# Performance work log

Hardware: AMD Instinct MI355X
Metric: run time of the kernel (lower is better)

## Reference

```python
import jax, jax.numpy as jnp
import numpy as np

C = 1024      # channels
K = 7         # kernel_size
G = 1         # groups (G>1 crashes in the original torch code; see notes)
GC = C // G   # group_channels
OFFSET_SCALE = 2.0
LN_EPS = 1e-5


def setup_inputs() -> dict:
    key = jax.random.key(0)
    ks = jax.random.split(key, 8)
    N, L = 4, 2048
    s = 1.0 / np.sqrt(C)
    x = jax.random.normal(ks[0], (N, L, C), jnp.float32)
    Wi = jax.random.normal(ks[1], (C, C), jnp.float32) * s
    bi = jnp.zeros((C,), jnp.float32)
    dw_w = jax.random.normal(ks[2], (C, 1, 3), jnp.float32) * 0.5   # depthwise conv kernel (O, I/g=1, W)
    dw_b = jnp.zeros((C,), jnp.float32)
    ln_g = jnp.ones((C,), jnp.float32)
    ln_b = jnp.zeros((C,), jnp.float32)
    Wo = jax.random.normal(ks[3], (G * K, C), jnp.float32) * 0.02   # offset head (nonzero to exercise gather)
    bo = jnp.zeros((G * K,), jnp.float32)
    Wm = jax.random.normal(ks[4], (G * K, C), jnp.float32) * 0.02   # mask head
    bm = jnp.zeros((G * K,), jnp.float32)
    Wout = jax.random.normal(ks[5], (C, C), jnp.float32) * s
    bout = jnp.zeros((C,), jnp.float32)
    return {"x": x, "Wi": Wi, "bi": bi, "dw_w": dw_w, "dw_b": dw_b,
            "ln_g": ln_g, "ln_b": ln_b, "Wo": Wo, "bo": bo,
            "Wm": Wm, "bm": bm, "Wout": Wout, "bout": bout}


def _forward(x, Wi, bi, dw_w, dw_b, ln_g, ln_b, Wo, bo, Wm, bm, Wout, bout):
    N, L, Cc = x.shape
    dt = x.dtype
    # input projection
    x_proj = x @ Wi.T + bi                                  # [N,L,C]
    # depthwise conv (k=3, pad=1, groups=C) -> LayerNorm(C) -> GELU(exact)
    y = jax.lax.conv_general_dilated(
        x.transpose(0, 2, 1), dw_w, window_strides=(1,), padding=((1, 1),),
        dimension_numbers=("NCH", "OIH", "NCH"), feature_group_count=Cc)
    x_dw = y.transpose(0, 2, 1) + dw_b                       # [N,L,C]
    mu = x_dw.mean(-1, keepdims=True)
    var = ((x_dw - mu) ** 2).mean(-1, keepdims=True)
    x_dw = (x_dw - mu) * jax.lax.rsqrt(var + LN_EPS) * ln_g + ln_b
    x_dw = jax.nn.gelu(x_dw, approximate=False)
    # dynamic offsets and sampling mask
    offsets = (x_dw @ Wo.T + bo).reshape(N, L, G, K) * OFFSET_SCALE
    mask = jax.nn.softmax((x_dw @ Wm.T + bm).reshape(N, L, G, K), axis=-1)
    mask = jnp.nan_to_num(mask, nan=0.0)
    # absolute sampling positions
    ref_off = jnp.linspace(-(K // 2), K // 2, K).astype(dt)          # [K]
    pos = jnp.arange(L, dtype=dt)[None, :, None, None]               # [1,L,1,1]
    abs_pos = pos + ref_off[None, None, None, :] + offsets           # [N,L,G,K]
    apc = jnp.clip(abs_pos, 0.0, L - 1)
    p_floor = jnp.clip(apc.astype(jnp.int32), 0, L - 1)
    p_ceil = jnp.clip(p_floor + 1, 0, L - 1)
    w_ceil = apc - p_floor.astype(dt)
    w_floor = 1.0 - w_ceil
    valid = jnp.logical_not((abs_pos < 0) | (abs_pos > L - 1)).astype(dt)
    w_floor = w_floor * valid
    w_ceil = w_ceil * valid
    # gather + bilinear blend (G=1: each sample index grabs the full C channels)
    idx_f = p_floor.reshape(N, -1)[:, :, None]                       # [N, L*G*K, 1]
    idx_c = p_ceil.reshape(N, -1)[:, :, None]
    v_floor = jnp.take_along_axis(x_proj, idx_f, axis=1).reshape(N, L, G, K, GC)
    v_ceil = jnp.take_along_axis(x_proj, idx_c, axis=1).reshape(N, L, G, K, GC)
    sampled = v_floor * w_floor[..., None] + v_ceil * w_ceil[..., None]
    out = (sampled * mask[..., None]).sum(axis=3).reshape(N, L, Cc)  # sum over K
    return out @ Wout.T + bout


def reference(x, Wi, bi, dw_w, dw_b, ln_g, ln_b, Wo, bo, Wm, bm, Wout, bout):
    return _forward(x, Wi, bi, dw_w, dw_b, ln_g, ln_b, Wo, bo, Wm, bm, Wout, bout)
```

## Files before the change

### kernel.cpp

```cpp
#include <hip/hip_runtime.h>
#include <hip/hip_bf16.h>
#include <cstdint>

#define C_DIM 1024
#define L_DIM 2048
#define N_DIM 4
#define M_DIM (N_DIM * L_DIM)

typedef __attribute__((ext_vector_type(8))) short frag8;
typedef __attribute__((ext_vector_type(4)))  float f32x4;
typedef __attribute__((ext_vector_type(16))) float f32x16;

__device__ __forceinline__ void gl_lds16(const void* g, void* l) {
  __builtin_amdgcn_global_load_lds((const __attribute__((address_space(1))) void*)g,
                                   (__attribute__((address_space(3))) void*)l,
                                   16, 0, 0);
}
__device__ __forceinline__ void store_out(float* Y, size_t idx, float v) { Y[idx] = v; }
__device__ __forceinline__ void store_out(__hip_bfloat16* Y, size_t idx, float v) {
  Y[idx] = __float2bfloat16(v);
}
__device__ __forceinline__ float4 ldbf4(const __hip_bfloat16* p) {
  union { short4 s; __hip_bfloat16 h[4]; } u; u.s = *(const short4*)p;
  return make_float4((float)u.h[0], (float)u.h[1], (float)u.h[2], (float)u.h[3]);
}
__device__ __forceinline__ void stbf4(__hip_bfloat16* p, float4 v) {
  union { short4 s; __hip_bfloat16 h[4]; } u;
  u.h[0] = __float2bfloat16(v.x); u.h[1] = __float2bfloat16(v.y);
  u.h[2] = __float2bfloat16(v.z); u.h[3] = __float2bfloat16(v.w);
  *(short4*)p = u.s;
}
__device__ __forceinline__ float gelu_fast(float t) {
  const float t3 = t * t * t;
  const float ns = -1.5957691216f * t - 0.0713548163f * t3;
  return t / (1.f + __expf(ns));
}

__global__ __launch_bounds__(256)
void cvt_f32_bf16(const float* __restrict__ in, __hip_bfloat16* __restrict__ out, int n8) {
  const int i = blockIdx.x * 256 + threadIdx.x;
  if (i >= n8) return;
  const float4 a = *(const float4*)(in + (size_t)i * 8);
  const float4 b = *(const float4*)(in + (size_t)i * 8 + 4);
  union { __hip_bfloat16 h[8]; int4 q; } u;
  u.h[0] = __float2bfloat16(a.x); u.h[1] = __float2bfloat16(a.y);
  u.h[2] = __float2bfloat16(a.z); u.h[3] = __float2bfloat16(a.w);
  u.h[4] = __float2bfloat16(b.x); u.h[5] = __float2bfloat16(b.y);
  u.h[6] = __float2bfloat16(b.z); u.h[7] = __float2bfloat16(b.w);
  *(int4*)(out + (size_t)i * 8) = u.q;
}

__global__ __launch_bounds__(256)
void cvt_two_f32_bf16(const float* __restrict__ inA, __hip_bfloat16* __restrict__ outA,
                      const float* __restrict__ inB, __hip_bfloat16* __restrict__ outB,
                      int n8each) {
  int i = blockIdx.x * 256 + threadIdx.x;
  const float* in; __hip_bfloat16* out;
  if (i < n8each) { in = inA; out = outA; }
  else            { in = inB; out = outB; i -= n8each; }
  if (i >= n8each) return;
  const float4 a = *(const float4*)(in + (size_t)i * 8);
  const float4 b = *(const float4*)(in + (size_t)i * 8 + 4);
  union { __hip_bfloat16 h[8]; int4 q; } u;
  u.h[0] = __float2bfloat16(a.x); u.h[1] = __float2bfloat16(a.y);
  u.h[2] = __float2bfloat16(a.z); u.h[3] = __float2bfloat16(a.w);
  u.h[4] = __float2bfloat16(b.x); u.h[5] = __float2bfloat16(b.y);
  u.h[6] = __float2bfloat16(b.z); u.h[7] = __float2bfloat16(b.w);
  *(int4*)(out + (size_t)i * 8) = u.q;
}

template <typename TY>
__global__ __launch_bounds__(256, 2)
void gemm_db(const __hip_bfloat16* __restrict__ X,
             const __hip_bfloat16* __restrict__ W,
             const float* __restrict__ bias,
             TY* __restrict__ Y, int M, int N, int K,
             const float* __restrict__ sArr, const float* __restrict__ bvec)
{
  __shared__ __hip_bfloat16 As[2][2][128 * 32];
  __shared__ __hip_bfloat16 Bs[2][2][128 * 32];
  const int tid  = threadIdx.x;
  const int lane = tid & 63;
  const int wave = tid >> 6;
  const int bm = blockIdx.x * 128;
  const int bn = blockIdx.y * 128;
  const int wr = (wave >> 1) * 64;
  const int wc = (wave & 1) * 64;
  const int srow  = tid >> 2;
  const int skoff = (tid & 3) * 8;

  const __hip_bfloat16* gA0 = X + (size_t)(bm + srow) * K + skoff;
  const __hip_bfloat16* gA1 = X + (size_t)(bm + 64 + srow) * K + skoff;
  const __hip_bfloat16* gB0 = W + (size_t)(bn + srow) * K + skoff;
  const __hip_bfloat16* gB1 = W + (size_t)(bn + 64 + srow) * K + skoff;

  f32x16 acc[2][2] = {};
  const int arow  = lane & 31;
  const int akoff = (lane >> 5) * 8;

#define STAGE(k0, buf)                                        \
  do {                                                        \
    gl_lds16(gA0 + (k0),      &As[buf][0][tid * 8]);          \
    gl_lds16(gA1 + (k0),      &As[buf][0][2048 + tid * 8]);   \
    gl_lds16(gA0 + (k0) + 32, &As[buf][1][tid * 8]);          \
    gl_lds16(gA1 + (k0) + 32, &As[buf][1][2048 + tid * 8]);   \
    gl_lds16(gB0 + (k0),      &Bs[buf][0][tid * 8]);          \
    gl_lds16(gB1 + (k0),      &Bs[buf][0][2048 + tid * 8]);   \
    gl_lds16(gB0 + (k0) + 32, &Bs[buf][1][tid * 8]);          \
    gl_lds16(gB1 + (k0) + 32, &Bs[buf][1][2048 + tid * 8]);   \
  } while (0)

  STAGE(0, 0);
  __syncthreads();
  const int iters = K / 64;
  for (int it = 0; it < iters; ++it) {
    const int cur = it & 1;
    if (it + 1 < iters) STAGE((it + 1) * 64, cur ^ 1);

#pragma unroll
    for (int p = 0; p < 2; ++p)
#pragma unroll
      for (int h = 0; h < 2; ++h) {
        const frag8 a0 = *(const frag8*)&As[cur][p][(wr + arow) * 32 + h * 16 + akoff];
        const frag8 a1 = *(const frag8*)&As[cur][p][(wr + 32 + arow) * 32 + h * 16 + akoff];
        const frag8 b0 = *(const frag8*)&Bs[cur][p][(wc + arow) * 32 + h * 16 + akoff];
        const frag8 b1 = *(const frag8*)&Bs[cur][p][(wc + 32 + arow) * 32 + h * 16 + akoff];
        acc[0][0] = __builtin_amdgcn_mfma_f32_32x32x16_bf16(a0, b0, acc[0][0], 0, 0, 0);
        acc[0][1] = __builtin_amdgcn_mfma_f32_32x32x16_bf16(a0, b1, acc[0][1], 0, 0, 0);
        acc[1][0] = __builtin_amdgcn_mfma_f32_32x32x16_bf16(a1, b0, acc[1][0], 0, 0, 0);
        acc[1][1] = __builtin_amdgcn_mfma_f32_32x32x16_bf16(a1, b1, acc[1][1], 0, 0, 0);
      }
    __syncthreads();
  }
#undef STAGE

#pragma unroll
  for (int i = 0; i < 2; i++)
#pragma unroll
    for (int j = 0; j < 2; j++) {
      const int col = bn + wc + j * 32 + (lane & 31);
      const float bv  = bias ? bias[col] : 0.f;
      const float bvv = (sArr && bvec) ? bvec[col] : 0.f;
#pragma unroll
      for (int r = 0; r < 16; r++) {
        const int row = bm + wr + i * 32 + (r & 3) + 8 * (r >> 2) + 4 * (lane >> 5);
        float extra = bv;
        if (sArr) extra += sArr[row] * bvv;
        store_out(Y, (size_t)row * N + col, acc[i][j][r] + extra);
      }
    }
}

struct Ld8f { float4 a, b; };
struct Ld8b { int4 a; };
__device__ __forceinline__ Ld8f ld8(const float* p) {
  return { *(const float4*)p, *(const float4*)(p + 4) };
}
__device__ __forceinline__ Ld8b ld8(const __hip_bfloat16* p) { return { *(const int4*)p }; }
__device__ __forceinline__ void st8(__hip_bfloat16* l, const Ld8f& v) {
  union { __hip_bfloat16 h[8]; int4 q; } u;
  u.h[0] = __float2bfloat16(v.a.x); u.h[1] = __float2bfloat16(v.a.y);
  u.h[2] = __float2bfloat16(v.a.z); u.h[3] = __float2bfloat16(v.a.w);
  u.h[4] = __float2bfloat16(v.b.x); u.h[5] = __float2bfloat16(v.b.y);
  u.h[6] = __float2bfloat16(v.b.z); u.h[7] = __float2bfloat16(v.b.w);
  *(int4*)l = u.q;
}
__device__ __forceinline__ void st8(__hip_bfloat16* l, const Ld8b& v) { *(int4*)l = v.a; }

template <typename TX, typename TY>
__global__ __launch_bounds__(256, 2)
void gemm_nt(const TX* __restrict__ X, const float* __restrict__ W,
             const float* __restrict__ bias, TY* __restrict__ Y, int M, int N, int K)
{
  __shared__ __hip_bfloat16 As[128 * 32];
  __shared__ __hip_bfloat16 Bs[128 * 32];
  const int tid  = threadIdx.x;
  const int lane = tid & 63;
  const int wave = tid >> 6;
  const int bm = blockIdx.x * 128;
  const int bn = blockIdx.y * 128;
  const int wr = (wave >> 1) * 64;
  const int wc = (wave & 1) * 64;
  const int srow  = tid >> 2;
  const int skoff = (tid & 3) * 8;

  f32x4 acc[4][4] = {};
  const TX*    gA0 = X + (size_t)(bm + srow) * K + skoff;
  const TX*    gA1 = X + (size_t)(bm + 64 + srow) * K + skoff;
  const float* gB0 = W + (size_t)(bn + srow) * K + skoff;
  const float* gB1 = W + (size_t)(bn + 64 + srow) * K + skoff;
  const int arow  = lane & 15;
  const int akoff = (lane >> 4) * 8;

  for (int k0 = 0; k0 < K; k0 += 32) {
    const auto va0 = ld8(gA0 + k0);
    const auto va1 = ld8(gA1 + k0);
    const auto vb0 = ld8(gB0 + k0);
    const auto vb1 = ld8(gB1 + k0);
    __syncthreads();
    st8(&As[srow * 32 + skoff],        va0);
    st8(&As[(64 + srow) * 32 + skoff], va1);
    st8(&Bs[srow * 32 + skoff],        vb0);
    st8(&Bs[(64 + srow) * 32 + skoff], vb1);
    __syncthreads();

    frag8 a[4], b[4];
#pragma unroll
    for (int i = 0; i < 4; i++)
      a[i] = *(const frag8*)&As[(wr + i * 16 + arow) * 32 + akoff];
#pragma unroll
    for (int j = 0; j < 4; j++)
      b[j] = *(const frag8*)&Bs[(wc + j * 16 + arow) * 32 + akoff];
#pragma unroll
    for (int i = 0; i < 4; i++)
#pragma unroll
      for (int j = 0; j < 4; j++)
        acc[i][j] = __builtin_amdgcn_mfma_f32_16x16x32_bf16(a[i], b[j], acc[i][j], 0, 0, 0);
  }
#pragma unroll
  for (int i = 0; i < 4; i++)
#pragma unroll
    for (int j = 0; j < 4; j++) {
      const int col = bn + wc + j * 16 + (lane & 15);
      const float bv = bias[col];
#pragma unroll
      for (int r = 0; r < 4; r++) {
        const int row = bm + wr + i * 16 + (lane >> 4) * 4 + r;
        store_out(Y, (size_t)row * N + col, acc[i][j][r] + bv);
      }
    }
}

__global__ __launch_bounds__(256, 2)
void pre_aux(const float* __restrict__ x,
             const float* __restrict__ dw_w, const float* __restrict__ dw_b,
             const float* __restrict__ ln_g, const float* __restrict__ ln_b,
             const float* __restrict__ Wo,   const float* __restrict__ bo,
             const float* __restrict__ Wm,   const float* __restrict__ bmb,
             const float* __restrict__ Wi,   const float* __restrict__ Wout,
             const float* __restrict__ bi,
             __hip_bfloat16* __restrict__ xbb,
             float* __restrict__ coef,
             __hip_bfloat16* __restrict__ WiT,
             __hip_bfloat16* __restrict__ Woutb,
             float* __restrict__ bvec)
{
  __shared__ float smem[16384];
  const int blk  = blockIdx.x;
  const int tid  = threadIdx.x;
  const int lane = tid & 63;
  const int wid  = tid >> 6;

  if (blk < 256) {
    float (*tile)[65] = (float(*)[65])smem;
    const int bi_ = blk >> 4;
    const int bj  = blk & 15;
    const int r   = tid >> 2;
    const int c0  = (tid & 3) * 16;
    const float* src = Wi + (size_t)(bi_ * 64 + r) * C_DIM + bj * 64 + c0;
    *(float4*)&tile[r][c0]      = *(const float4*)(src);
    *(float4*)&tile[r][c0 + 4]  = *(const float4*)(src + 4);
    *(float4*)&tile[r][c0 + 8]  = *(const float4*)(src + 8);
    *(float4*)&tile[r][c0 + 12] = *(const float4*)(src + 12);
    __syncthreads();
    __hip_bfloat16* dst = WiT + (size_t)(bj * 64 + r) * C_DIM + bi_ * 64 + c0;
    union { __hip_bfloat16 h[16]; int4 q[2]; } u;
#pragma unroll
    for (int i = 0; i < 16; i++) u.h[i] = __float2bfloat16(tile[c0 + i][r]);
    *(int4*)(dst)     = u.q[0];
    *(int4*)(dst + 8) = u.q[1];
    return;
  }
  if (blk < 512) {
    const size_t base = ((size_t)(blk - 256) * 256 + tid) * 16;
#pragma unroll
    for (int h = 0; h < 2; h++) {
      const float4 a = *(const float4*)(Wout + base + h * 8);
      const float4 c = *(const float4*)(Wout + base + h * 8 + 4);
      union { __hip_bfloat16 h8[8]; int4 q; } u;
      u.h8[0] = __float2bfloat16(a.x); u.h8[1] = __float2bfloat16(a.y);
      u.h8[2] = __float2bfloat16(a.z); u.h8[3] = __float2bfloat16(a.w);
      u.h8[4] = __float2bfloat16(c.x); u.h8[5] = __float2bfloat16(c.y);
      u.h8[6] = __float2bfloat16(c.z); u.h8[7] = __float2bfloat16(c.w);
      *(int4*)(Woutb + base + h * 8) = u.q;
    }
    return;
  }
  if (blk < 768) {
    const int row = (blk - 512) * 4 + wid;
    const float* wr_ = Wout + (size_t)row * C_DIM;
    float s = 0.f;
#pragma unroll
    for (int c = 0; c < 4; c++) {
      const int j = c * 256 + lane * 4;
      const float4 w  = *(const float4*)(wr_ + j);
      const float4 bb = *(const float4*)(bi + j);
      s += w.x * bb.x + w.y * bb.y + w.z * bb.z + w.w * bb.w;
    }
#pragma unroll
    for (int m = 1; m < 64; m <<= 1) s += __shfl_xor(s, m);
    if (lane == 0) bvec[row] = s;
    return;
  }

  float* sWo  = smem;
  float* sWm  = smem + 7168;
  float* slng = smem + 14336;
  float* slnb = smem + 15360;

#pragma unroll
  for (int i = 0; i < 7; i++)
    gl_lds16(Wo + (size_t)(i * 256 + tid) * 4, &sWo[(i * 256 + tid) * 4]);
#pragma unroll
  for (int i = 0; i < 7; i++)
    gl_lds16(Wm + (size_t)(i * 256 + tid) * 4, &sWm[(i * 256 + tid) * 4]);
  gl_lds16(ln_g + (size_t)tid * 4, &slng[tid * 4]);
  gl_lds16(ln_b + (size_t)tid * 4, &slnb[tid * 4]);
  __syncthreads();

  const int b    = blk - 768;
  const int bs   = (b & 7) * 64 + (b >> 3);
  const int row0 = bs * 16 + wid * 4;
  const int l0   = row0 & (L_DIM - 1);

  const float* xr = x + (size_t)row0 * C_DIM;

  float4 v[4][4];
#pragma unroll
  for (int j = 0; j < 4; j++) {
    const int c4 = j * 256 + lane * 4;
    float4 xv[6];
#pragma unroll
    for (int m = 0; m < 6; m++) {
      const int lm = l0 + m - 1;
      if (lm >= 0 && lm < L_DIM)
        xv[m] = *(const float4*)(xr + ((long)m - 1) * C_DIM + c4);
      else
        xv[m] = make_float4(0.f, 0.f, 0.f, 0.f);
    }
#pragma unroll
    for (int r = 0; r < 4; r++)
      stbf4(xbb + (size_t)(row0 + r) * C_DIM + c4, xv[r + 1]);

    const float4 w0 = *(const float4*)(dw_w + (size_t)c4 * 3);
    const float4 w1 = *(const float4*)(dw_w + (size_t)c4 * 3 + 4);
    const float4 w2 = *(const float4*)(dw_w + (size_t)c4 * 3 + 8);
    const float4 bb = *(const float4*)(dw_b + c4);
#pragma unroll
    for (int r = 0; r < 4; r++) {
      const float4 xm = xv[r], x0 = xv[r + 1], xq = xv[r + 2];
      v[r][j].x = xm.x * w0.x + x0.x * w0.y + xq.x * w0.z + bb.x;
      v[r][j].y = xm.y * w0.w + x0.y * w1.x + xq.y * w1.y + bb.y;
      v[r][j].z = xm.z * w1.z + x0.z * w1.w + xq.z * w2.x + bb.z;
      v[r][j].w = xm.w * w2.y + x0.w * w2.z + xq.w * w2.w + bb.w;
    }
  }

  float mu[4], rstd[4];
#pragma unroll
  for (int r = 0; r < 4; r++) {
    float s1 = 0.f, s2 = 0.f;
#pragma unroll
    for (int j = 0; j < 4; j++) {
      s1 += v[r][j].x + v[r][j].y + v[r][j].z + v[r][j].w;
      s2 += v[r][j].x * v[r][j].x + v[r][j].y * v[r][j].y
          + v[r][j].z * v[r][j].z + v[r][j].w * v[r][j].w;
    }
    const float t1 = s1 + __shfl_xor(s1, 32);
    const float t2 = s2 + __shfl_xor(s2, 32);
    float cc = (lane < 32) ? t1 : t2;
#pragma unroll
    for (int m = 16; m >= 1; m >>= 1) cc += __shfl_xor(cc, m);
    const float dd = __shfl_xor(cc, 32);
    const float S1 = (lane < 32) ? cc : dd;
    const float S2 = (lane < 32) ? dd : cc;
    mu[r]   = S1 * (1.f / C_DIM);
    rstd[r] = rsqrtf(S2 * (1.f / C_DIM) - mu[r] * mu[r] + 1e-5f);
  }

  float po[4][7] = {}, pm[4][7] = {};
#pragma unroll
  for (int j = 0; j < 4; j++) {
    const int c4 = j * 256 + lane * 4;
    const float4 gg = *(const float4*)&slng[c4];
    const float4 bb = *(const float4*)&slnb[c4];
    float4 g[4];
#pragma unroll
    for (int r = 0; r < 4; r++) {
      g[r].x = gelu_fast((v[r][j].x - mu[r]) * rstd[r] * gg.x + bb.x);
      g[r].y = gelu_fast((v[r][j].y - mu[r]) * rstd[r] * gg.y + bb.y);
      g[r].z = gelu_fast((v[r][j].z - mu[r]) * rstd[r] * gg.z + bb.z);
      g[r].w = gelu_fast((v[r][j].w - mu[r]) * rstd[r] * gg.w + bb.w);
    }
#pragma unroll
    for (int k = 0; k < 7; k++) {
      const float4 wo = *(const float4*)&sWo[k * 1024 + c4];
      const float4 wm = *(const float4*)&sWm[k * 1024 + c4];
#pragma unroll
      for (int r = 0; r < 4; r++) {
        po[r][k] += g[r].x * wo.x + g[r].y * wo.y + g[r].z * wo.z + g[r].w * wo.w;
        pm[r][k] += g[r].x * wm.x + g[r].y * wm.y + g[r].z * wm.z + g[r].w * wm.w;
      }
    }
  }

  float poS[4][7], pmS[4][7];
#pragma unroll
  for (int r = 0; r < 4; r++)
#pragma unroll
    for (int k = 0; k < 7; k++) {
      const float tp = po[r][k] + __shfl_xor(po[r][k], 32);
      const float tm = pm[r][k] + __shfl_xor(pm[r][k], 32);
      float cc = (lane < 32) ? tp : tm;
#pragma unroll
      for (int m = 16; m >= 1; m >>= 1) cc += __shfl_xor(cc, m);
      const float dd = __shfl_xor(cc, 32);
      poS[r][k] = (lane < 32) ? cc : dd;
      pmS[r][k] = (lane < 32) ? dd : cc;
    }

#pragma unroll
  for (int r = 0; r < 4; r++) {
    float lg[7], mx = -1e30f;
#pragma unroll
    for (int k = 0; k < 7; k++) { lg[k] = pmS[r][k] + bmb[k]; mx = fmaxf(mx, lg[k]); }
    float se = 0.f, e[7];
#pragma unroll
    for (int k = 0; k < 7; k++) { e[k] = __expf(lg[k] - mx); se += e[k]; }
    const float inv = 1.f / se;
    const int l = l0 + r;

    if (lane == r) {
      float pk[32];
#pragma unroll
      for (int k = 0; k < 7; k++) {
        const float msk = e[k] * inv;
        const float off = (poS[r][k] + bo[k]) * 2.0f;
        const float ap  = (float)l + (float)(k - 3) + off;
        const float apc = fminf(fmaxf(ap, 0.f), (float)(L_DIM - 1));
        int f = (int)apc;
        int c = f + 1; if (c > L_DIM - 1) c = L_DIM - 1;
        const float w1  = apc - (float)f;
        const float val = (ap < 0.f || ap > (float)(L_DIM - 1)) ? 0.f : 1.f;
        pk[k]      = (1.f - w1) * val * msk;
        pk[8 + k]  = w1 * val * msk;
        pk[16 + k] = (float)f;
        pk[24 + k] = (float)c;
      }
      pk[7] = pk[15] = pk[23] = pk[31] = 0.f;
      float* cr = coef + (size_t)(row0 + r) * 32;
#pragma unroll
      for (int q = 0; q < 8; q++)
        *(float4*)(cr + q * 4) = make_float4(pk[q*4], pk[q*4+1], pk[q*4+2], pk[q*4+3]);
    }
  }
}

__global__ __launch_bounds__(512, 2)
void wcomb_gather(const __hip_bfloat16* __restrict__ Woutb,
                  const __hip_bfloat16* __restrict__ WiT,
                  __hip_bfloat16* __restrict__ Wcb,
                  const float* __restrict__ coef,
                  const __hip_bfloat16* __restrict__ xbb,
                  __hip_bfloat16* __restrict__ gb,
                  float* __restrict__ sArr)
{
  __shared__ __hip_bfloat16 As[2][2][128 * 32];
  __shared__ __hip_bfloat16 Bs[2][2][128 * 32];
  const int tid  = threadIdx.x;
  const int lane = tid & 63;
  const int wid  = tid >> 6;

  if (blockIdx.x < 64) {
    if (wid >= 4) {
      for (int i = 0; i < 17; i++) __syncthreads();
      return;
    }
    const int bm = (int)(blockIdx.x >> 3) * 128;
    const int bn = (int)(blockIdx.x & 7) * 128;
    const int wr = (wid >> 1) * 64;
    const int wc = (wid & 1) * 64;
    const int srow  = tid >> 2;
    const int skoff = (tid & 3) * 8;
    const int K = C_DIM;

    const __hip_bfloat16* gA0 = Woutb + (size_t)(bm + srow) * K + skoff;
    const __hip_bfloat16* gA1 = Woutb + (size_t)(bm + 64 + srow) * K + skoff;
    const __hip_bfloat16* gB0 = WiT   + (size_t)(bn + srow) * K + skoff;
    const __hip_bfloat16* gB1 = WiT   + (size_t)(bn + 64 + srow) * K + skoff;

    f32x16 acc[2][2] = {};
    const int arow  = lane & 31;
    const int akoff = (lane >> 5) * 8;

#define WSTAGE(k0, buf)                                       \
  do {                                                        \
    gl_lds16(gA0 + (k0),      &As[buf][0][tid * 8]);          \
    gl_lds16(gA1 + (k0),      &As[buf][0][2048 + tid * 8]);   \
    gl_lds16(gA0 + (k0) + 32, &As[buf][1][tid * 8]);          \
    gl_lds16(gA1 + (k0) + 32, &As[buf][1][2048 + tid * 8]);   \
    gl_lds16(gB0 + (k0),      &Bs[buf][0][tid * 8]);          \
    gl_lds16(gB1 + (k0),      &Bs[buf][0][2048 + tid * 8]);   \
    gl_lds16(gB0 + (k0) + 32, &Bs[buf][1][tid * 8]);          \
    gl_lds16(gB1 + (k0) + 32, &Bs[buf][1][2048 + tid * 8]);   \
  } while (0)

    WSTAGE(0, 0);
    __syncthreads();
    for (int it = 0; it < 16; ++it) {
      const int cur = it & 1;
      if (it + 1 < 16) WSTAGE((it + 1) * 64, cur ^ 1);
#pragma unroll
      for (int p = 0; p < 2; ++p)
#pragma unroll
        for (int h = 0; h < 2; ++h) {
          const frag8 a0 = *(const frag8*)&As[cur][p][(wr + arow) * 32 + h * 16 + akoff];
          const frag8 a1 = *(const frag8*)&As[cur][p][(wr + 32 + arow) * 32 + h * 16 + akoff];
          const frag8 b0 = *(const frag8*)&Bs[cur][p][(wc + arow) * 32 + h * 16 + akoff];
          const frag8 b1 = *(const frag8*)&Bs[cur][p][(wc + 32 + arow) * 32 + h * 16 + akoff];
          acc[0][0] = __builtin_amdgcn_mfma_f32_32x32x16_bf16(a0, b0, acc[0][0], 0, 0, 0);
          acc[0][1] = __builtin_amdgcn_mfma_f32_32x32x16_bf16(a0, b1, acc[0][1], 0, 0, 0);
          acc[1][0] = __builtin_amdgcn_mfma_f32_32x32x16_bf16(a1, b0, acc[1][0], 0, 0, 0);
          acc[1][1] = __builtin_amdgcn_mfma_f32_32x32x16_bf16(a1, b1, acc[1][1], 0, 0, 0);
        }
      __syncthreads();
    }
#undef WSTAGE

#pragma unroll
    for (int i = 0; i < 2; i++)
#pragma unroll
      for (int j = 0; j < 2; j++) {
        const int col = bn + wc + j * 32 + (lane & 31);
#pragma unroll
        for (int r = 0; r < 16; r++) {
          const int row = bm + wr + i * 32 + (r & 3) + 8 * (r >> 2) + 4 * (lane >> 5);
          Wcb[(size_t)row * C_DIM + col] = __float2bfloat16(acc[i][j][r]);
        }
      }
    return;
  }

  const int b   = (int)blockIdx.x - 64;
  const int bs  = (b & 7) * 128 + (b >> 3);
  const int row = bs * 8 + wid;
  const int n   = row >> 11;

  const float* cr = coef + (size_t)row * 32;
  const float4 q0 = *(const float4*)(cr);
  const float4 q1 = *(const float4*)(cr + 4);
  const float4 q2 = *(const float4*)(cr + 8);
  const float4 q3 = *(const float4*)(cr + 12);
  const float4 q4 = *(const float4*)(cr + 16);
  const float4 q5 = *(const float4*)(cr + 20);
  const float4 q6 = *(const float4*)(cr + 24);
  const float4 q7 = *(const float4*)(cr + 28);

  const float wf[7] = {q0.x, q0.y, q0.z, q0.w, q1.x, q1.y, q1.z};
  const float wc[7] = {q2.x, q2.y, q2.z, q2.w, q3.x, q3.y, q3.z};
  const int   pf[7] = {(int)q4.x, (int)q4.y, (int)q4.z, (int)q4.w, (int)q5.x, (int)q5.y, (int)q5.z};
  const int   pc[7] = {(int)q6.x, (int)q6.y, (int)q6.z, (int)q6.w, (int)q7.x, (int)q7.y, (int)q7.z};

  if (lane == 0) {
    sArr[row] = q0.x + q0.y + q0.z + q0.w + q1.x + q1.y + q1.z
              + q2.x + q2.y + q2.z + q2.w + q3.x + q3.y + q3.z;
  }

  const __hip_bfloat16* xpn = xbb + ((size_t)n * L_DIM) * C_DIM;
  __hip_bfloat16* so = gb + (size_t)row * C_DIM;

#pragma unroll
  for (int j = 0; j < 2; j++) {
    const int c8 = j * 512 + lane * 8;
    float a[8] = {0.f, 0.f, 0.f, 0.f, 0.f, 0.f, 0.f, 0.f};
#pragma unroll
    for (int k = 0; k < 7; k++) {
      union { int4 q; __hip_bfloat16 h[8]; } uf, uc;
      uf.q = *(const int4*)(xpn + (size_t)pf[k] * C_DIM + c8);
      uc.q = *(const int4*)(xpn + (size_t)pc[k] * C_DIM + c8);
#pragma unroll
      for (int t = 0; t < 8; t++)
        a[t] += wf[k] * (float)uf.h[t] + wc[k] * (float)uc.h[t];
    }
    union { int4 q; __hip_bfloat16 h[8]; } uo;
#pragma unroll
    for (int t = 0; t < 8; t++) uo.h[t] = __float2bfloat16(a[t]);
    *(int4*)(so + c8) = uo.q;
  }
}

__global__ __launch_bounds__(256)
void mid_fused_v4(const float* __restrict__ x,
                  const float* __restrict__ dw_w, const float* __restrict__ dw_b,
                  const float* __restrict__ ln_g, const float* __restrict__ ln_b,
                  const float* __restrict__ Wo,   const float* __restrict__ bo,
                  const float* __restrict__ Wm,   const float* __restrict__ bmb,
                  const __hip_bfloat16* __restrict__ xp,
                  __hip_bfloat16* __restrict__ smp)
{
  const int b    = blockIdx.x;
  const int bs   = (b & 7) * 256 + (b >> 3);
  const int wid  = threadIdx.x >> 6;
  const int lane = threadIdx.x & 63;
  const int row  = bs * 4 + wid;
  const int l    = row & (L_DIM - 1);
  const int n    = row >> 11;

  const float* xr = x + (size_t)row * C_DIM;

  float4 v[4];
#pragma unroll
  for (int j = 0; j < 4; j++) {
    const int c4 = j * 256 + lane * 4;
    const float4 x0 = *(const float4*)(xr + c4);
    float4 xm = make_float4(0.f, 0.f, 0.f, 0.f);
    float4 xq = make_float4(0.f, 0.f, 0.f, 0.f);
    if (l > 0)         xm = *(const float4*)(xr + c4 - C_DIM);
    if (l < L_DIM - 1) xq = *(const float4*)(xr + c4 + C_DIM);
    const float4 w0 = *(const float4*)(dw_w + (size_t)c4 * 3);
    const float4 w1 = *(const float4*)(dw_w + (size_t)c4 * 3 + 4);
    const float4 w2 = *(const float4*)(dw_w + (size_t)c4 * 3 + 8);
    const float4 bb = *(const float4*)(dw_b + c4);
    v[j].x = xm.x * w0.x + x0.x * w0.y + xq.x * w0.z + bb.x;
    v[j].y = xm.y * w0.w + x0.y * w1.x + xq.y * w1.y + bb.y;
    v[j].z = xm.z * w1.z + x0.z * w1.w + xq.z * w2.x + bb.z;
    v[j].w = xm.w * w2.y + x0.w * w2.z + xq.w * w2.w + bb.w;
  }

  float s1 = 0.f, s2 = 0.f;
#pragma unroll
  for (int j = 0; j < 4; j++) {
    s1 += v[j].x + v[j].y + v[j].z + v[j].w;
    s2 += v[j].x * v[j].x + v[j].y * v[j].y + v[j].z * v[j].z + v[j].w * v[j].w;
  }
#pragma unroll
  for (int m = 1; m < 64; m <<= 1) { s1 += __shfl_xor(s1, m); s2 += __shfl_xor(s2, m); }
  const float mu   = s1 * (1.f / C_DIM);
  const float rstd = rsqrtf(s2 * (1.f / C_DIM) - mu * mu + 1e-5f);

  float4 g[4];
#pragma unroll
  for (int j = 0; j < 4; j++) {
    const int c4 = j * 256 + lane * 4;
    const float4 gg = *(const float4*)(ln_g + c4);
    const float4 bb = *(const float4*)(ln_b + c4);
    g[j].x = gelu_fast((v[j].x - mu) * rstd * gg.x + bb.x);
    g[j].y = gelu_fast((v[j].y - mu) * rstd * gg.y + bb.y);
    g[j].z = gelu_fast((v[j].z - mu) * rstd * gg.z + bb.z);
    g[j].w = gelu_fast((v[j].w - mu) * rstd * gg.w + bb.w);
  }

  float po[7] = {0,0,0,0,0,0,0}, pm[7] = {0,0,0,0,0,0,0};
#pragma unroll
  for (int k = 0; k < 7; k++) {
#pragma unroll
    for (int j = 0; j < 4; j++) {
      const int c4 = j * 256 + lane * 4;
      const float4 wo = *(const float4*)(Wo + (size_t)k * C_DIM + c4);
      const float4 wm = *(const float4*)(Wm + (size_t)k * C_DIM + c4);
      po[k] += g[j].x * wo.x + g[j].y * wo.y + g[j].z * wo.z + g[j].w * wo.w;
      pm[k] += g[j].x * wm.x + g[j].y * wm.y + g[j].z * wm.z + g[j].w * wm.w;
    }
  }
#pragma unroll
  for (int k = 0; k < 7; k++)
#pragma unroll
    for (int m = 1; m < 64; m <<= 1) {
      po[k] += __shfl_xor(po[k], m);
      pm[k] += __shfl_xor(pm[k], m);
    }

  float lg[7], mx = -1e30f;
#pragma unroll
  for (int k = 0; k < 7; k++) { lg[k] = pm[k] + bmb[k]; mx = fmaxf(mx, lg[k]); }
  float se = 0.f, e[7];
#pragma unroll
  for (int k = 0; k < 7; k++) { e[k] = __expf(lg[k] - mx); se += e[k]; }
  const float inv = 1.f / se;

  float wf[7], wcl[7]; int pf[7], pc[7];
#pragma unroll
  for (int k = 0; k < 7; k++) {
    const float msk = e[k] * inv;
    const float off = (po[k] + bo[k]) * 2.0f;
    const float ap  = (float)l + (float)(k - 3) + off;
    const float apc = fminf(fmaxf(ap, 0.f), (float)(L_DIM - 1));
    int f = (int)apc;
    int c = f + 1; if (c > L_DIM - 1) c = L_DIM - 1;
    const float w1  = apc - (float)f;
    const float val = (ap < 0.f || ap > (float)(L_DIM - 1)) ? 0.f : 1.f;
    wf[k]  = (1.f - w1) * val * msk;
    wcl[k] = w1 * val * msk;
    pf[k] = f; pc[k] = c;
  }

  const __hip_bfloat16* xpn = xp + ((size_t)n * L_DIM) * C_DIM;
  __hip_bfloat16* so = smp + (size_t)row * C_DIM;
#pragma unroll
  for (int j = 0; j < 4; j++) {
    const int c4 = j * 256 + lane * 4;
    float4 a = make_float4(0.f, 0.f, 0.f, 0.f);
#pragma unroll
    for (int k = 0; k < 7; k++) {
      const float4 vf = ldbf4(xpn + (size_t)pf[k] * C_DIM + c4);
      const float4 vc = ldbf4(xpn + (size_t)pc[k] * C_DIM + c4);
      a.x += wf[k] * vf.x + wcl[k] * vc.x;
      a.y += wf[k] * vf.y + wcl[k] * vc.y;
      a.z += wf[k] * vf.z + wcl[k] * vc.z;
      a.w += wf[k] * vf.w + wcl[k] * vc.w;
    }
    stbf4(so + c4, a);
  }
}

extern "C" void kernel_launch(void* const* d_in, const int* in_sizes, int n_in,
                              void* d_out, int out_size, void* d_ws, size_t ws_size,
                              hipStream_t stream)
{
  const float* x    = (const float*)d_in[0];
  const float* Wi   = (const float*)d_in[1];
  const float* bi   = (const float*)d_in[2];
  const float* dw_w = (const float*)d_in[3];
  const float* dw_b = (const float*)d_in[4];
  const float* ln_g = (const float*)d_in[5];
  const float* ln_b = (const float*)d_in[6];
  const float* Wo   = (const float*)d_in[7];
  const float* bo   = (const float*)d_in[8];
  const float* Wm   = (const float*)d_in[9];
  const float* bm   = (const float*)d_in[10];
  const float* Wout = (const float*)d_in[11];
  const float* bout = (const float*)d_in[12];
  float* out = (float*)d_out;

  const size_t XE = (size_t)M_DIM * C_DIM;
  const size_t WE = (size_t)C_DIM * C_DIM;
  char* wsb = (char*)d_ws;

  __hip_bfloat16* xbb2  = (__hip_bfloat16*)wsb;
  __hip_bfloat16* gb    = (__hip_bfloat16*)(wsb + XE * 2);
  __hip_bfloat16* Woutb2= (__hip_bfloat16*)(wsb + XE * 4);
  __hip_bfloat16* WiT   = (__hip_bfloat16*)(wsb + XE * 4 + WE * 2);
  __hip_bfloat16* Wcb   = (__hip_bfloat16*)(wsb + XE * 4 + WE * 4);
  float* coef2 = (float*)(wsb + XE * 4 + WE * 6);
  float* sArr  = (float*)(wsb + XE * 4 + WE * 6 + (size_t)M_DIM * 128);
  float* bvec  = (float*)(wsb + XE * 4 + WE * 6 + (size_t)M_DIM * 128 + (size_t)M_DIM * 4);
  const size_t need_v5 = XE * 4 + WE * 6 + (size_t)M_DIM * 132 + 4096;

  __hip_bfloat16* xp    = (__hip_bfloat16*)wsb;
  __hip_bfloat16* smp   = (__hip_bfloat16*)(wsb + XE * 2);
  __hip_bfloat16* Wib   = (__hip_bfloat16*)(wsb + XE * 4);
  __hip_bfloat16* Woutb = (__hip_bfloat16*)(wsb + XE * 4 + WE * 2);
  __hip_bfloat16* xbb   = (__hip_bfloat16*)(wsb + XE * 4 + WE * 4);
  const size_t need_w2   = XE * 4 + WE * 4;
  const size_t need_full = need_w2 + XE * 2;

  dim3 gg(M_DIM / 128, C_DIM / 128);

  if (ws_size >= need_v5) {
    pre_aux<<<1280, 256, 0, stream>>>(
        x, dw_w, dw_b, ln_g, ln_b, Wo, bo, Wm, bm,
        Wi, Wout, bi, xbb2, coef2, WiT, Woutb2, bvec);
    wcomb_gather<<<1088, 512, 0, stream>>>(
        Woutb2, WiT, Wcb, coef2, xbb2, gb, sArr);
    gemm_db<float><<<gg, 256, 0, stream>>>(
        gb, Wcb, bout, out, M_DIM, C_DIM, C_DIM, sArr, bvec);
  } else if (ws_size >= need_full) {
    cvt_f32_bf16<<<(int)(XE / 8 / 256), 256, 0, stream>>>(x, xbb, (int)(XE / 8));
    cvt_two_f32_bf16<<<(int)(2 * (WE / 8) / 256), 256, 0, stream>>>(
        Wi, Wib, Wout, Woutb, (int)(WE / 8));
    gemm_db<__hip_bfloat16><<<gg, 256, 0, stream>>>(xbb, Wib, bi, xp, M_DIM, C_DIM, C_DIM,
                                                    nullptr, nullptr);
    mid_fused_v4<<<M_DIM / 4, 256, 0, stream>>>(x, dw_w, dw_b, ln_g, ln_b, Wo, bo, Wm, bm, xp, smp);
    gemm_db<float><<<gg, 256, 0, stream>>>(smp, Woutb, bout, out, M_DIM, C_DIM, C_DIM,
                                           nullptr, nullptr);
  } else if (ws_size >= need_w2) {
    cvt_f32_bf16<<<(int)(WE / 8 / 256), 256, 0, stream>>>(Wout, Woutb, (int)(WE / 8));
    gemm_nt<float, __hip_bfloat16><<<gg, 256, 0, stream>>>(x, Wi, bi, xp, M_DIM, C_DIM, C_DIM);
    mid_fused_v4<<<M_DIM / 4, 256, 0, stream>>>(x, dw_w, dw_b, ln_g, ln_b, Wo, bo, Wm, bm, xp, smp);
    gemm_db<float><<<gg, 256, 0, stream>>>(smp, Woutb, bout, out, M_DIM, C_DIM, C_DIM,
                                           nullptr, nullptr);
  } else {
    gemm_nt<float, __hip_bfloat16><<<gg, 256, 0, stream>>>(x, Wi, bi, xp, M_DIM, C_DIM, C_DIM);
    mid_fused_v4<<<M_DIM / 4, 256, 0, stream>>>(x, dw_w, dw_b, ln_g, ln_b, Wo, bo, Wm, bm, xp, smp);
    gemm_nt<__hip_bfloat16, float><<<gg, 256, 0, stream>>>(smp, Wout, bout, out, M_DIM, C_DIM, C_DIM);
  }
}
```

Before: 180.5 us.

## Shrink fused weight-combine/gather kernel to 256-thread blocks with smaller K stage

The fused kernel that multiplies Wout by Wi and also runs the row gather now uses 256-thread blocks instead of 512. The 64 GEMM blocks no longer leave half their waves idle on barriers, and their K stage shrinks from 64 to 32, cutting shared memory per block in half. Gather blocks now cover 4 rows each instead of 8, so the grid doubles to 2112 blocks. The aim is better occupancy and less waste in the GEMM blocks, at the cost of twice as many K-loop iterations and barriers.

Measured after the change: 180.6 us. Within noise of the previous version (+0.0%).

```diff
diff --git a/kernel.cpp b/kernel.cpp
--- a/kernel.cpp
+++ b/kernel.cpp
@@ -456,76 +456,62 @@
   }
 }
 
-__global__ __launch_bounds__(512, 2)
-void wcomb_gather(const __hip_bfloat16* __restrict__ Woutb,
-                  const __hip_bfloat16* __restrict__ WiT,
-                  __hip_bfloat16* __restrict__ Wcb,
-                  const float* __restrict__ coef,
-                  const __hip_bfloat16* __restrict__ xbb,
-                  __hip_bfloat16* __restrict__ gb,
-                  float* __restrict__ sArr)
+__global__ __launch_bounds__(256, 2)
+void wcomb_gather2(const __hip_bfloat16* __restrict__ Woutb,
+                   const __hip_bfloat16* __restrict__ WiT,
+                   __hip_bfloat16* __restrict__ Wcb,
+                   const float* __restrict__ coef,
+                   const __hip_bfloat16* __restrict__ xbb,
+                   __hip_bfloat16* __restrict__ gb,
+                   float* __restrict__ sArr)
 {
-  __shared__ __hip_bfloat16 As[2][2][128 * 32];
-  __shared__ __hip_bfloat16 Bs[2][2][128 * 32];
+  __shared__ __hip_bfloat16 sm[2][2][128 * 32];
   const int tid  = threadIdx.x;
   const int lane = tid & 63;
   const int wid  = tid >> 6;
 
   if (blockIdx.x < 64) {
-    if (wid >= 4) {
-      for (int i = 0; i < 17; i++) __syncthreads();
-      return;
-    }
     const int bm = (int)(blockIdx.x >> 3) * 128;
     const int bn = (int)(blockIdx.x & 7) * 128;
     const int wr = (wid >> 1) * 64;
     const int wc = (wid & 1) * 64;
-    const int srow  = tid >> 2;
-    const int skoff = (tid & 3) * 8;
-    const int K = C_DIM;
-
-    const __hip_bfloat16* gA0 = Woutb + (size_t)(bm + srow) * K + skoff;
-    const __hip_bfloat16* gA1 = Woutb + (size_t)(bm + 64 + srow) * K + skoff;
-    const __hip_bfloat16* gB0 = WiT   + (size_t)(bn + srow) * K + skoff;
-    const __hip_bfloat16* gB1 = WiT   + (size_t)(bn + 64 + srow) * K + skoff;
+    const int K  = C_DIM;
+    const int r0  = tid >> 2;
+    const int kc0 = (tid & 3) * 8;
+    const __hip_bfloat16* gA = Woutb + (size_t)bm * K;
+    const __hip_bfloat16* gB = WiT   + (size_t)bn * K;
+
+#define W2STAGE(k0, buf)                                                          \
+    do {                                                                          \
+      gl_lds16(gA + (size_t)r0 * K + (k0) + kc0,        &sm[buf][0][tid * 8]);    \
+      gl_lds16(gA + (size_t)(r0 + 64) * K + (k0) + kc0, &sm[buf][0][2048 + tid * 8]); \
+      gl_lds16(gB + (size_t)r0 * K + (k0) + kc0,        &sm[buf][1][tid * 8]);    \
+      gl_lds16(gB + (size_t)(r0 + 64) * K + (k0) + kc0, &sm[buf][1][2048 + tid * 8]); \
+    } while (0)
 
     f32x16 acc[2][2] = {};
     const int arow  = lane & 31;
     const int akoff = (lane >> 5) * 8;
 
-#define WSTAGE(k0, buf)                                       \
-  do {                                                        \
-    gl_lds16(gA0 + (k0),      &As[buf][0][tid * 8]);          \
-    gl_lds16(gA1 + (k0),      &As[buf][0][2048 + tid * 8]);   \
-    gl_lds16(gA0 + (k0) + 32, &As[buf][1][tid * 8]);          \
-    gl_lds16(gA1 + (k0) + 32, &As[buf][1][2048 + tid * 8]);   \
-    gl_lds16(gB0 + (k0),      &Bs[buf][0][tid * 8]);          \
-    gl_lds16(gB1 + (k0),      &Bs[buf][0][2048 + tid * 8]);   \
-    gl_lds16(gB0 + (k0) + 32, &Bs[buf][1][tid * 8]);          \
-    gl_lds16(gB1 + (k0) + 32, &Bs[buf][1][2048 + tid * 8]);   \
-  } while (0)
-
-    WSTAGE(0, 0);
+    W2STAGE(0, 0);
     __syncthreads();
-    for (int it = 0; it < 16; ++it) {
+    for (int it = 0; it < 32; ++it) {
       const int cur = it & 1;
-      if (it + 1 < 16) WSTAGE((it + 1) * 64, cur ^ 1);
-#pragma unroll
-      for (int p = 0; p < 2; ++p)
-#pragma unroll
-        for (int h = 0; h < 2; ++h) {
-          const frag8 a0 = *(const frag8*)&As[cur][p][(wr + arow) * 32 + h * 16 + akoff];
-          const frag8 a1 = *(const frag8*)&As[cur][p][(wr + 32 + arow) * 32 + h * 16 + akoff];
-          const frag8 b0 = *(const frag8*)&Bs[cur][p][(wc + arow) * 32 + h * 16 + akoff];
-          const frag8 b1 = *(const frag8*)&Bs[cur][p][(wc + 32 + arow) * 32 + h * 16 + akoff];
-          acc[0][0] = __builtin_amdgcn_mfma_f32_32x32x16_bf16(a0, b0, acc[0][0], 0, 0, 0);
-          acc[0][1] = __builtin_amdgcn_mfma_f32_32x32x16_bf16(a0, b1, acc[0][1], 0, 0, 0);
-          acc[1][0] = __builtin_amdgcn_mfma_f32_32x32x16_bf16(a1, b0, acc[1][0], 0, 0, 0);
-          acc[1][1] = __builtin_amdgcn_mfma_f32_32x32x16_bf16(a1, b1, acc[1][1], 0, 0, 0);
-        }
+      if (it + 1 < 32) W2STAGE((it + 1) * 32, cur ^ 1);
+#pragma unroll
+      for (int h = 0; h < 2; ++h) {
+        const frag8 a0 = *(const frag8*)&sm[cur][0][(wr + arow) * 32 + h * 16 + akoff];
+        const frag8 a1 = *(const frag8*)&sm[cur][0][(wr + 32 + arow) * 32 + h * 16 + akoff];
+        const frag8 b0 = *(const frag8*)&sm[cur][1][(wc + arow) * 32 + h * 16 + akoff];
+        const frag8 b1 = *(const frag8*)&sm[cur][1][(wc + 32 + arow) * 32 + h * 16 + akoff];
+        acc[0][0] = __builtin_amdgcn_mfma_f32_32x32x16_bf16(a0, b0, acc[0][0], 0, 0, 0);
+        acc[0][1] = __builtin_amdgcn_mfma_f32_32x32x16_bf16(a0, b1, acc[0][1], 0, 0, 0);
+        acc[1][0] = __builtin_amdgcn_mfma_f32_32x32x16_bf16(a1, b0, acc[1][0], 0, 0, 0);
+        acc[1][1] = __builtin_amdgcn_mfma_f32_32x32x16_bf16(a1, b1, acc[1][1], 0, 0, 0);
+      }
       __syncthreads();
     }
-#undef WSTAGE
+#undef W2STAGE
 
 #pragma unroll
     for (int i = 0; i < 2; i++)
@@ -542,8 +528,8 @@
   }
 
   const int b   = (int)blockIdx.x - 64;
-  const int bs  = (b & 7) * 128 + (b >> 3);
-  const int row = bs * 8 + wid;
+  const int bs  = (b & 7) * 256 + (b >> 3);
+  const int row = bs * 4 + wid;
   const int n   = row >> 11;
 
   const float* cr = coef + (size_t)row * 32;
@@ -760,7 +746,7 @@
     pre_aux<<<1280, 256, 0, stream>>>(
         x, dw_w, dw_b, ln_g, ln_b, Wo, bo, Wm, bm,
         Wi, Wout, bi, xbb2, coef2, WiT, Woutb2, bvec);
-    wcomb_gather<<<1088, 512, 0, stream>>>(
+    wcomb_gather2<<<2112, 256, 0, stream>>>(
         Woutb2, WiT, Wcb, coef2, xbb2, gb, sArr);
     gemm_db<float><<<gg, 256, 0, stream>>>(
         gb, Wcb, bout, out, M_DIM, C_DIM, C_DIM, sArr, bvec);
```
